# Kernel tuning notes

Hardware: AMD Instinct MI355X
Metric: run time of the kernel (lower is better)

The kernel has to match this reference:

```python
import jax, jax.numpy as jnp
import numpy as np

N_NODES = 100000
N_EDGES = 1600000
N_GRAPHS = 64
BN_EPS = 1e-5


def setup_inputs() -> dict:
    key = jax.random.key(0)
    ks = jax.random.split(key, 16)
    inp = {
        'x': jax.random.normal(ks[0], (N_NODES, 768), dtype=jnp.float32),
        'edge_index': jax.random.randint(ks[1], (2, N_EDGES), 0, N_NODES, dtype=jnp.int32),
        'batch': jnp.sort(jax.random.randint(ks[2], (N_NODES,), 0, N_GRAPHS, dtype=jnp.int32)),
        'W_in': jax.random.normal(ks[3], (768, 256), dtype=jnp.float32) * 0.02,
        'b_in': jax.random.normal(ks[4], (256,), dtype=jnp.float32) * 0.02,
        'W_g': jax.random.normal(ks[5], (3, 256, 256), dtype=jnp.float32) * 0.05,
        'b_g': jax.random.normal(ks[6], (3, 256), dtype=jnp.float32) * 0.02,
        'bn_gamma': jax.random.uniform(ks[7], (3, 256), dtype=jnp.float32) + 0.5,
        'bn_beta': jax.random.normal(ks[8], (3, 256), dtype=jnp.float32) * 0.02,
        'bn_mean': jax.random.normal(ks[9], (3, 256), dtype=jnp.float32) * 0.02,
        'bn_var': jax.random.uniform(ks[10], (3, 256), dtype=jnp.float32) + 0.5,
        'W1': jax.random.normal(ks[11], (256, 128), dtype=jnp.float32) * 0.06,
        'b1': jax.random.normal(ks[12], (128,), dtype=jnp.float32) * 0.02,
        'W2': jax.random.normal(ks[13], (128, 128), dtype=jnp.float32) * 0.08,
        'b2': jax.random.normal(ks[14], (128,), dtype=jnp.float32) * 0.02,
    }
    return inp


def reference(x, edge_index, batch, W_in, b_in, W_g, b_g, bn_gamma, bn_beta,
              bn_mean, bn_var, W1, b1, W2, b2):
    N = x.shape[0]
    # Add self loops (PyG GCNConv default)
    loop = jnp.arange(N, dtype=edge_index.dtype)
    src = jnp.concatenate([edge_index[0], loop])  # [E+N]
    dst = jnp.concatenate([edge_index[1], loop])
    # Symmetric GCN normalization: deg over dst after self loops
    deg = jax.ops.segment_sum(jnp.ones_like(src, dtype=x.dtype), dst, num_segments=N)
    dinv = jnp.where(deg > 0, jax.lax.rsqrt(deg), 0.0)
    norm = (dinv[src] * dinv[dst])[:, None]  # [E+N, 1]

    # input projection + relu
    h = jax.nn.relu(x @ W_in + b_in)  # [N, 256]

    for i in range(W_g.shape[0]):
        m = h @ W_g[i]                                   # [N, 256]
        agg = jax.ops.segment_sum(m[src] * norm, dst, num_segments=N) + b_g[i]
        # BatchNorm (eval mode, running stats)
        agg = (agg - bn_mean[i]) * (bn_gamma[i] * jax.lax.rsqrt(bn_var[i] + BN_EPS)) + bn_beta[i]
        h = jax.nn.relu(agg)  # dropout is identity in eval

    # global mean pool per graph
    sums = jax.ops.segment_sum(h, batch, num_segments=N_GRAPHS)       # [G, 256]
    cnts = jax.ops.segment_sum(jnp.ones((N,), x.dtype), batch, num_segments=N_GRAPHS)
    g = sums / jnp.maximum(cnts, 1.0)[:, None]

    # output MLP
    out = jax.nn.relu(g @ W1 + b1) @ W2 + b2  # [G, 128]
    return out
```

## Files before the change

kernel.cpp:

```cpp
#include <hip/hip_runtime.h>
#include <hip/hip_fp16.h>

#define HIDDEN 256

using hfrag = __attribute__((ext_vector_type(8))) _Float16;
using facc16 = __attribute__((ext_vector_type(16))) float;

#define BARRIER_LGKM()                                   \
  do {                                                   \
    asm volatile("s_waitcnt lgkmcnt(0)" ::: "memory");   \
    __builtin_amdgcn_s_barrier();                        \
  } while (0)

__device__ inline float h2f(unsigned short h) {
  return __half2float(__builtin_bit_cast(__half, h));
}
__device__ inline unsigned short f2h_bits(float v) {
  return __builtin_bit_cast(unsigned short, __float2half(v));
}
__device__ inline hfrag f2h8(const float4& a, const float4& b) {
  hfrag h;
  h[0] = (_Float16)a.x; h[1] = (_Float16)a.y;
  h[2] = (_Float16)a.z; h[3] = (_Float16)a.w;
  h[4] = (_Float16)b.x; h[5] = (_Float16)b.y;
  h[6] = (_Float16)b.z; h[7] = (_Float16)b.w;
  return h;
}

__global__ __launch_bounds__(256) void k_scan_a(const int* __restrict__ deg,
                                                int* __restrict__ bsum, int N) {
  const int t = threadIdx.x, lane = t & 63, w = t >> 6;
  const int idx = blockIdx.x * 256 + t;
  int x = (idx < N) ? deg[idx] : 0;
#pragma unroll
  for (int off = 32; off >= 1; off >>= 1) x += __shfl_xor(x, off);
  __shared__ int ws[4];
  if (lane == 0) ws[w] = x;
  __syncthreads();
  if (t == 0) bsum[blockIdx.x] = ws[0] + ws[1] + ws[2] + ws[3];
}

__global__ __launch_bounds__(512) void k_scan_b(const int* __restrict__ bsum,
                                                int* __restrict__ boff, int nb) {
  const int t = threadIdx.x, lane = t & 63, w = t >> 6;
  int orig = (t < nb) ? bsum[t] : 0;
  int x = orig;
#pragma unroll
  for (int off = 1; off < 64; off <<= 1) {
    int y = __shfl_up(x, off);
    if (lane >= off) x += y;
  }
  __shared__ int wsum[8];
  if (lane == 63) wsum[w] = x;
  __syncthreads();
  if (w == 0 && lane < 8) {
    int s = wsum[lane];
#pragma unroll
    for (int off = 1; off < 8; off <<= 1) {
      int y = __shfl_up(s, off);
      if (lane >= off) s += y;
    }
    wsum[lane] = s;
  }
  __syncthreads();
  int inc = x + (w > 0 ? wsum[w - 1] : 0);
  if (t < nb) boff[t] = inc - orig;
}

__global__ __launch_bounds__(256) void k_scan_c(const int* __restrict__ deg,
                                                const int* __restrict__ boff,
                                                int* __restrict__ row_ptr,
                                                float* __restrict__ dinv, int N) {
  const int t = threadIdx.x, lane = t & 63, w = t >> 6;
  const int idx = blockIdx.x * 256 + t;
  int d = (idx < N) ? deg[idx] : 0;
  int x = d;
#pragma unroll
  for (int off = 1; off < 64; off <<= 1) {
    int y = __shfl_up(x, off);
    if (lane >= off) x += y;
  }
  __shared__ int ws[4];
  if (lane == 63) ws[w] = x;
  __syncthreads();
  int add = boff[blockIdx.x];
#pragma unroll
  for (int j = 0; j < 4; ++j)
    if (j < w) add += ws[j];
  if (idx < N) {
    row_ptr[idx + 1] = x + add;
    dinv[idx] = 1.0f / sqrtf((float)d + 1.0f);
  }
  if (idx == 0) row_ptr[0] = 0;
}

__global__ __launch_bounds__(256) void k_prep_w(const float* __restrict__ W_in,
                                                const float* __restrict__ W_g,
                                                short* __restrict__ Wt) {
  const int e = blockIdx.x * blockDim.x + threadIdx.x;
  if (e >= 196608 + 3 * 65536) return;
  float v;
  int k, n;
  size_t base;
  if (e < 196608) {
    k = e >> 8;
    n = e & 255;
    v = W_in[e];
    base = 0;
  } else {
    int r = e - 196608;
    int lyr = r >> 16;
    k = (r >> 8) & 255;
    n = r & 255;
    v = W_g[r];
    base = 393216 + (size_t)lyr * 131072;
  }
  size_t pos = base + (size_t)(k >> 5) * 16384 + (size_t)n * 32 + (k & 31);
  __half hh = __float2half(v);
  float r2 = v - __half2float(hh);
  Wt[pos] = (short)__builtin_bit_cast(unsigned short, hh);
  Wt[pos + 8192] = (short)__builtin_bit_cast(unsigned short, __float2half(r2));
}

__device__ __forceinline__ void proj_body(int bx, const float* __restrict__ A,
                                          const short* __restrict__ Wt,
                                          const float* __restrict__ bias,
                                          unsigned short* __restrict__ Ch,
                                          int M, int K) {
  __shared__ short As[2][64][34];
  const int t = threadIdx.x;
  const int w = t >> 6, l = t & 63;
  const int g2 = l >> 5, l31 = l & 31;
  const int row0 = bx * 64;
  const int colbase = w * 64;
  const int arow = t >> 2, ak = (t & 3) << 3;

  facc16 acc[2][2];
#pragma unroll
  for (int i = 0; i < 2; ++i)
#pragma unroll
    for (int j = 0; j < 2; ++j) acc[i][j] = (facc16)(0.0f);

  const int nsteps = K >> 5;
  const int ga = row0 + arow;
  const bool aval = ga < M;
  const float* aptr = A + (size_t)ga * K + ak;

  float4 f0 = make_float4(0.f, 0.f, 0.f, 0.f), f1 = f0;
  if (aval) {
    f0 = *(const float4*)aptr;
    f1 = *(const float4*)(aptr + 4);
  }
  *(hfrag*)&As[0][arow][ak] = f2h8(f0, f1);
  if (nsteps > 1 && aval) {
    f0 = *(const float4*)(aptr + 32);
    f1 = *(const float4*)(aptr + 36);
  }

  int cur = 0;
  for (int s = 0; s < nsteps; ++s) {
    BARRIER_LGKM();
    hfrag bh[2][2], bl[2][2];
#pragma unroll
    for (int nt = 0; nt < 2; ++nt)
#pragma unroll
      for (int kh = 0; kh < 2; ++kh) {
        const short* wbp = Wt + ((size_t)s << 14) +
                           (size_t)(colbase + nt * 32 + l31) * 32 + kh * 16 + g2 * 8;
        bh[nt][kh] = *(const hfrag*)wbp;
        bl[nt][kh] = *(const hfrag*)(wbp + 8192);
      }
#pragma unroll
    for (int kh = 0; kh < 2; ++kh) {
      hfrag ah[2];
#pragma unroll
      for (int mt = 0; mt < 2; ++mt)
        ah[mt] = *(const hfrag*)&As[cur][mt * 32 + l31][kh * 16 + g2 * 8];
#pragma unroll
      for (int mt = 0; mt < 2; ++mt)
#pragma unroll
        for (int nt = 0; nt < 2; ++nt)
          acc[mt][nt] = __builtin_amdgcn_mfma_f32_32x32x16_f16(
              ah[mt], bh[nt][kh], acc[mt][nt], 0, 0, 0);
#pragma unroll
      for (int mt = 0; mt < 2; ++mt)
#pragma unroll
        for (int nt = 0; nt < 2; ++nt)
          acc[mt][nt] = __builtin_amdgcn_mfma_f32_32x32x16_f16(
              ah[mt], bl[nt][kh], acc[mt][nt], 0, 0, 0);
    }
    if (s + 1 < nsteps) {
      *(hfrag*)&As[cur ^ 1][arow][ak] = f2h8(f0, f1);
      if (s + 2 < nsteps && aval) {
        const float* ap = aptr + (size_t)(s + 2) * 32;
        f0 = *(const float4*)(ap + 0);
        f1 = *(const float4*)(ap + 4);
      }
    }
    cur ^= 1;
  }
#pragma unroll
  for (int nt = 0; nt < 2; ++nt) {
    const int col = colbase + nt * 32 + l31;
    const float b = bias[col];
#pragma unroll
    for (int mt = 0; mt < 2; ++mt)
#pragma unroll
      for (int r = 0; r < 16; ++r) {
        int row = row0 + mt * 32 + (r & 3) + 8 * (r >> 2) + 4 * g2;
        if (row < M)
          Ch[(size_t)row * HIDDEN + col] = f2h_bits(fmaxf(acc[mt][nt][r] + b, 0.f));
      }
  }
}

#define LG_LOAD(S, AA, BH, BL)                                          \
  {                                                                     \
    AA[0][0] = *(const hfrag*)(ap0 + (S) * 32);                         \
    AA[0][1] = *(const hfrag*)(ap0 + (S) * 32 + 16);                    \
    AA[1][0] = *(const hfrag*)(ap1 + (S) * 32);                         \
    AA[1][1] = *(const hfrag*)(ap1 + (S) * 32 + 16);                    \
    const short* wp = wb + ((size_t)(S) << 14);                         \
    BH[0][0] = *(const hfrag*)(wp);                                     \
    BH[0][1] = *(const hfrag*)(wp + 16);                                \
    BH[1][0] = *(const hfrag*)(wp + 1024);                              \
    BH[1][1] = *(const hfrag*)(wp + 1024 + 16);                         \
    BL[0][0] = *(const hfrag*)(wp + 8192);                              \
    BL[0][1] = *(const hfrag*)(wp + 8192 + 16);                         \
    BL[1][0] = *(const hfrag*)(wp + 8192 + 1024);                       \
    BL[1][1] = *(const hfrag*)(wp + 8192 + 1024 + 16);                  \
  }

#define LG_COMPUTE(AA, BH, BL)                                          \
  _Pragma("unroll") for (int kh = 0; kh < 2; ++kh) {                    \
    _Pragma("unroll") for (int mt = 0; mt < 2; ++mt)                    \
        _Pragma("unroll") for (int nt = 0; nt < 2; ++nt) acc[mt][nt] =  \
        __builtin_amdgcn_mfma_f32_32x32x16_f16(AA[mt][kh], BH[nt][kh],  \
                                               acc[mt][nt], 0, 0, 0);   \
    _Pragma("unroll") for (int mt = 0; mt < 2; ++mt)                    \
        _Pragma("unroll") for (int nt = 0; nt < 2; ++nt) acc[mt][nt] =  \
        __builtin_amdgcn_mfma_f32_32x32x16_f16(AA[mt][kh], BL[nt][kh],  \
                                               acc[mt][nt], 0, 0, 0);   \
  }

__device__ __forceinline__ void layer_gemm_body(
    int bx, const unsigned short* __restrict__ A, const short* __restrict__ Wt,
    const float* __restrict__ dinv, unsigned short* __restrict__ Cm, int M) {
  const int t = threadIdx.x;
  const int w = t >> 6, l = t & 63;
  const int g2 = l >> 5, l31 = l & 31;
  const int row0 = bx * 64;
  const int colbase = w * 64;

  facc16 acc[2][2];
#pragma unroll
  for (int i = 0; i < 2; ++i)
#pragma unroll
    for (int j = 0; j < 2; ++j) acc[i][j] = (facc16)(0.0f);

  int r0 = row0 + l31, r1 = row0 + 32 + l31;
  if (r0 >= M) r0 = M - 1;
  if (r1 >= M) r1 = M - 1;
  const unsigned short* ap0 = A + (size_t)r0 * HIDDEN + g2 * 8;
  const unsigned short* ap1 = A + (size_t)r1 * HIDDEN + g2 * 8;
  const short* wb = Wt + (size_t)(colbase + l31) * 32 + g2 * 8;

  hfrag aA[2][2], bhA[2][2], blA[2][2];
  hfrag aB[2][2], bhB[2][2], blB[2][2];

  LG_LOAD(0, aA, bhA, blA);
#pragma unroll
  for (int s = 0; s < 8; s += 2) {
    if (s + 1 < 8) LG_LOAD(s + 1, aB, bhB, blB);
    LG_COMPUTE(aA, bhA, blA);
    if (s + 2 < 8) LG_LOAD(s + 2, aA, bhA, blA);
    LG_COMPUTE(aB, bhB, blB);
  }
#pragma unroll
  for (int mt = 0; mt < 2; ++mt)
#pragma unroll
    for (int r = 0; r < 16; ++r) {
      int row = row0 + mt * 32 + (r & 3) + 8 * (r >> 2) + 4 * g2;
      if (row >= M) continue;
      const float sc = dinv[row];
#pragma unroll
      for (int nt = 0; nt < 2; ++nt)
        Cm[(size_t)row * HIDDEN + colbase + nt * 32 + l31] =
            f2h_bits(acc[mt][nt][r] * sc);
    }
}

__global__ __launch_bounds__(256, 3) void k_mega1(
    const float* __restrict__ x, const short* __restrict__ Wt,
    const float* __restrict__ b_in, unsigned short* __restrict__ h0, int M,
    int K, const int* __restrict__ dst, int* __restrict__ deg, int E,
    int ngemm, int nhist) {
  if ((int)blockIdx.x < ngemm) {
    proj_body(blockIdx.x, x, Wt, b_in, h0, M, K);
  } else {
    const int b = blockIdx.x - ngemm;
    for (int e = b * 256 + threadIdx.x; e < E; e += nhist * 256)
      atomicAdd(&deg[dst[e]], 1);
  }
}

__global__ __launch_bounds__(256, 2) void k_mega2(
    const unsigned short* __restrict__ h0, const short* __restrict__ WtL,
    const float* __restrict__ dinv, unsigned short* __restrict__ h1, int M,
    const int* __restrict__ src, const int* __restrict__ dst,
    const int* __restrict__ row_ptr, int* __restrict__ fill,
    int* __restrict__ csr, int E, int ngemm, int nfill) {
  if ((int)blockIdx.x < ngemm) {
    layer_gemm_body(blockIdx.x, h0, WtL, dinv, h1, M);
  } else {
    const int b = blockIdx.x - ngemm;
    for (int e = b * 256 + threadIdx.x; e < E; e += nfill * 256) {
      int d = dst[e];
      int pos = atomicAdd(&fill[d], 1);
      csr[row_ptr[d] + pos] = src[e];
    }
  }
}

__global__ __launch_bounds__(256, 2) void k_gemm_layer(
    const unsigned short* __restrict__ h, const short* __restrict__ WtL,
    const float* __restrict__ dinv, unsigned short* __restrict__ m, int M) {
  layer_gemm_body(blockIdx.x, h, WtL, dinv, m, M);
}

__global__ __launch_bounds__(256) void k_aggregate(
    const unsigned short* __restrict__ mp, const int* __restrict__ row_ptr,
    const int* __restrict__ csr, const float* __restrict__ dinv,
    const float* __restrict__ bg, const float* __restrict__ gamma,
    const float* __restrict__ beta, const float* __restrict__ mean,
    const float* __restrict__ var, unsigned short* __restrict__ hout, int N) {
  const int wave = threadIdx.x >> 6, l = threadIdx.x & 63;
  const int v = blockIdx.x * 4 + wave;
  if (v >= N) return;
  const int co = l << 2;
  ushort4 rs = *(const ushort4*)(mp + (size_t)v * HIDDEN + co);
  float4 acc;
  acc.x = h2f(rs.x); acc.y = h2f(rs.y); acc.z = h2f(rs.z); acc.w = h2f(rs.w);
  const int s = row_ptr[v], e = row_ptr[v + 1];
  int i = s;
  for (; i + 8 <= e; i += 8) {
    ushort4 r0 = *(const ushort4*)(mp + (size_t)csr[i + 0] * HIDDEN + co);
    ushort4 r1 = *(const ushort4*)(mp + (size_t)csr[i + 1] * HIDDEN + co);
    ushort4 r2 = *(const ushort4*)(mp + (size_t)csr[i + 2] * HIDDEN + co);
    ushort4 r3 = *(const ushort4*)(mp + (size_t)csr[i + 3] * HIDDEN + co);
    ushort4 r4 = *(const ushort4*)(mp + (size_t)csr[i + 4] * HIDDEN + co);
    ushort4 r5 = *(const ushort4*)(mp + (size_t)csr[i + 5] * HIDDEN + co);
    ushort4 r6 = *(const ushort4*)(mp + (size_t)csr[i + 6] * HIDDEN + co);
    ushort4 r7 = *(const ushort4*)(mp + (size_t)csr[i + 7] * HIDDEN + co);
    acc.x += h2f(r0.x) + h2f(r1.x) + h2f(r2.x) + h2f(r3.x) +
             h2f(r4.x) + h2f(r5.x) + h2f(r6.x) + h2f(r7.x);
    acc.y += h2f(r0.y) + h2f(r1.y) + h2f(r2.y) + h2f(r3.y) +
             h2f(r4.y) + h2f(r5.y) + h2f(r6.y) + h2f(r7.y);
    acc.z += h2f(r0.z) + h2f(r1.z) + h2f(r2.z) + h2f(r3.z) +
             h2f(r4.z) + h2f(r5.z) + h2f(r6.z) + h2f(r7.z);
    acc.w += h2f(r0.w) + h2f(r1.w) + h2f(r2.w) + h2f(r3.w) +
             h2f(r4.w) + h2f(r5.w) + h2f(r6.w) + h2f(r7.w);
  }
  for (; i < e; ++i) {
    ushort4 r0 = *(const ushort4*)(mp + (size_t)csr[i] * HIDDEN + co);
    acc.x += h2f(r0.x);
    acc.y += h2f(r0.y);
    acc.z += h2f(r0.z);
    acc.w += h2f(r0.w);
  }
  const float dv = dinv[v];
  float4 bg4 = *(const float4*)&bg[co];
  float4 g4 = *(const float4*)&gamma[co];
  float4 be4 = *(const float4*)&beta[co];
  float4 mn4 = *(const float4*)&mean[co];
  float4 vr4 = *(const float4*)&var[co];
  ushort4 o;
  o.x = f2h_bits(fmaxf((acc.x * dv + bg4.x - mn4.x) * (g4.x / sqrtf(vr4.x + 1e-5f)) + be4.x, 0.f));
  o.y = f2h_bits(fmaxf((acc.y * dv + bg4.y - mn4.y) * (g4.y / sqrtf(vr4.y + 1e-5f)) + be4.y, 0.f));
  o.z = f2h_bits(fmaxf((acc.z * dv + bg4.z - mn4.z) * (g4.z / sqrtf(vr4.z + 1e-5f)) + be4.z, 0.f));
  o.w = f2h_bits(fmaxf((acc.w * dv + bg4.w - mn4.w) * (g4.w / sqrtf(vr4.w + 1e-5f)) + be4.w, 0.f));
  *(ushort4*)&hout[(size_t)v * HIDDEN + co] = o;
}

__global__ __launch_bounds__(64) void k_count(const int* __restrict__ batch,
                                              float* __restrict__ cnt, int N,
                                              int G) {
  const int g = threadIdx.x;
  if (g >= G) return;
  int lo = 0, hi = N;
  while (lo < hi) {
    int mid = (lo + hi) >> 1;
    if (batch[mid] < g) lo = mid + 1; else hi = mid;
  }
  int lo2 = lo, hi2 = N;
  while (lo2 < hi2) {
    int mid = (lo2 + hi2) >> 1;
    if (batch[mid] < g + 1) lo2 = mid + 1; else hi2 = mid;
  }
  cnt[g] = (float)(lo2 - lo);
}

__global__ __launch_bounds__(256) void k_pool(const unsigned short* __restrict__ h,
                                              const int* __restrict__ batch,
                                              float* __restrict__ sums, int N) {
  const int t = threadIdx.x;
  const int start = blockIdx.x * 256;
  if (start >= N) return;
  const int end = min(start + 256, N);
  float acc = 0.f;
  int cur = batch[start];
  for (int n = start; n < end; ++n) {
    int g = batch[n];
    if (g != cur) {
      atomicAdd(&sums[cur * HIDDEN + t], acc);
      acc = 0.f;
      cur = g;
    }
    acc += h2f(h[(size_t)n * HIDDEN + t]);
  }
  atomicAdd(&sums[cur * HIDDEN + t], acc);
}

__global__ __launch_bounds__(128) void k_head(const float* __restrict__ sums,
                                              const float* __restrict__ cnt,
                                              const float* __restrict__ W1,
                                              const float* __restrict__ b1,
                                              const float* __restrict__ W2,
                                              const float* __restrict__ b2,
                                              float* __restrict__ out) {
  __shared__ float gr[256];
  __shared__ float t1[128];
  const int b = blockIdx.x, t = threadIdx.x;
  const float inv = 1.0f / fmaxf(cnt[b], 1.0f);
  gr[t] = sums[b * HIDDEN + t] * inv;
  gr[t + 128] = sums[b * HIDDEN + t + 128] * inv;
  __syncthreads();
  float a = b1[t];
  for (int k = 0; k < 256; ++k) a += gr[k] * W1[k * 128 + t];
  t1[t] = fmaxf(a, 0.f);
  __syncthreads();
  float o = b2[t];
  for (int k = 0; k < 128; ++k) o += t1[k] * W2[k * 128 + t];
  out[b * 128 + t] = o;
}

extern "C" void kernel_launch(void* const* d_in, const int* in_sizes, int n_in,
                              void* d_out, int out_size, void* d_ws,
                              size_t ws_size, hipStream_t stream) {
  (void)n_in;
  (void)ws_size;
  const float* x = (const float*)d_in[0];
  const int* ei = (const int*)d_in[1];
  const int* batch = (const int*)d_in[2];
  const float* W_in = (const float*)d_in[3];
  const float* b_in = (const float*)d_in[4];
  const float* W_g = (const float*)d_in[5];
  const float* b_g = (const float*)d_in[6];
  const float* bn_gamma = (const float*)d_in[7];
  const float* bn_beta = (const float*)d_in[8];
  const float* bn_mean = (const float*)d_in[9];
  const float* bn_var = (const float*)d_in[10];
  const float* W1 = (const float*)d_in[11];
  const float* b1 = (const float*)d_in[12];
  const float* W2 = (const float*)d_in[13];
  const float* b2 = (const float*)d_in[14];

  const int KIN = 768;
  const int N = in_sizes[0] / KIN;
  const int E = in_sizes[1] / 2;
  const int G = out_size / 128;

  const int* src = ei;
  const int* dst = ei + E;

  char* ws = (char*)d_ws;
  size_t off = 0;
  auto take = [&](size_t bytes) -> void* {
    void* p = ws + off;
    off += (bytes + 255) & ~(size_t)255;
    return p;
  };
  unsigned short* h0 = (unsigned short*)take((size_t)N * HIDDEN * 2);
  unsigned short* h1 = (unsigned short*)take((size_t)N * HIDDEN * 2);
  float* dinv = (float*)take((size_t)N * 4);
  int* deg = (int*)take((size_t)N * 4);
  int* fill = (int*)take((size_t)N * 4);
  int* row_ptr = (int*)take((size_t)(N + 1) * 4);
  int* csr = (int*)take((size_t)E * 4);
  float* sums = (float*)take((size_t)G * HIDDEN * 4);
  float* cnt = (float*)take((size_t)G * 4);
  short* Wt = (short*)take((size_t)(393216 + 3 * 131072) * 2);
  const int nb = (N + 255) / 256;
  int* bsum = (int*)take((size_t)nb * 4);
  int* boff = (int*)take((size_t)nb * 4);

  hipMemsetAsync(deg, 0, (size_t)N * 4, stream);
  hipMemsetAsync(fill, 0, (size_t)N * 4, stream);
  hipMemsetAsync(sums, 0, (size_t)G * HIDDEN * 4, stream);

  const int gx = (N + 63) / 64;
  const int NH = 256;
  const int NF = 256;

  k_prep_w<<<(196608 + 3 * 65536 + 255) / 256, 256, 0, stream>>>(W_in, W_g, Wt);
  k_mega1<<<gx + NH, 256, 0, stream>>>(x, Wt, b_in, h0, N, KIN, dst, deg, E,
                                       gx, NH);
  k_scan_a<<<nb, 256, 0, stream>>>(deg, bsum, N);
  k_scan_b<<<1, 512, 0, stream>>>(bsum, boff, nb);
  k_scan_c<<<nb, 256, 0, stream>>>(deg, boff, row_ptr, dinv, N);
  k_mega2<<<gx + NF, 256, 0, stream>>>(h0, Wt + 393216, dinv, h1, N, src, dst,
                                       row_ptr, fill, csr, E, gx, NF);
  k_aggregate<<<(N + 3) / 4, 256, 0, stream>>>(
      h1, row_ptr, csr, dinv, b_g, bn_gamma, bn_beta, bn_mean, bn_var, h0, N);
  for (int i = 1; i < 3; ++i) {
    k_gemm_layer<<<gx, 256, 0, stream>>>(h0, Wt + 393216 + (size_t)i * 131072,
                                         dinv, h1, N);
    k_aggregate<<<(N + 3) / 4, 256, 0, stream>>>(
        h1, row_ptr, csr, dinv, b_g + i * HIDDEN, bn_gamma + i * HIDDEN,
        bn_beta + i * HIDDEN, bn_mean + i * HIDDEN, bn_var + i * HIDDEN, h0, N);
  }
  k_count<<<1, 64, 0, stream>>>(batch, cnt, N, G);
  k_pool<<<(N + 255) / 256, 256, 0, stream>>>(h0, batch, sums, N);
  k_head<<<G, 128, 0, stream>>>(sums, cnt, W1, b1, W2, b2, (float*)d_out);
}
```

Before: 974.9 us.

## Drop LDS staging in input projection; load x straight into MFMA fragments

The input projection GEMM no longer stages x through shared memory with a barrier every K-step. Each lane now loads its fp32 rows of x straight from global memory into registers, converts them to fp16 fragments, and double-buffers both A and B across a fully unrolled 24-step K loop. This removes the LDS round trip and the per-step barriers. In exchange it uses many more registers (raw float4 buffers for two stages), so launch bounds drop from 3 to 2 blocks per CU, which lowers occupancy. Each wave also loads x rows redundantly, since every one of the four waves reads the same A rows.

```diff
diff --git a/kernel.cpp b/kernel.cpp
--- a/kernel.cpp
+++ b/kernel.cpp
@@ -5,12 +5,6 @@
 
 using hfrag = __attribute__((ext_vector_type(8))) _Float16;
 using facc16 = __attribute__((ext_vector_type(16))) float;
-
-#define BARRIER_LGKM()                                   \
-  do {                                                   \
-    asm volatile("s_waitcnt lgkmcnt(0)" ::: "memory");   \
-    __builtin_amdgcn_s_barrier();                        \
-  } while (0)
 
 __device__ inline float h2f(unsigned short h) {
   return __half2float(__builtin_bit_cast(__half, h));
@@ -122,104 +116,8 @@
   Wt[pos + 8192] = (short)__builtin_bit_cast(unsigned short, __float2half(r2));
 }
 
-__device__ __forceinline__ void proj_body(int bx, const float* __restrict__ A,
-                                          const short* __restrict__ Wt,
-                                          const float* __restrict__ bias,
-                                          unsigned short* __restrict__ Ch,
-                                          int M, int K) {
-  __shared__ short As[2][64][34];
-  const int t = threadIdx.x;
-  const int w = t >> 6, l = t & 63;
-  const int g2 = l >> 5, l31 = l & 31;
-  const int row0 = bx * 64;
-  const int colbase = w * 64;
-  const int arow = t >> 2, ak = (t & 3) << 3;
-
-  facc16 acc[2][2];
-#pragma unroll
-  for (int i = 0; i < 2; ++i)
-#pragma unroll
-    for (int j = 0; j < 2; ++j) acc[i][j] = (facc16)(0.0f);
-
-  const int nsteps = K >> 5;
-  const int ga = row0 + arow;
-  const bool aval = ga < M;
-  const float* aptr = A + (size_t)ga * K + ak;
-
-  float4 f0 = make_float4(0.f, 0.f, 0.f, 0.f), f1 = f0;
-  if (aval) {
-    f0 = *(const float4*)aptr;
-    f1 = *(const float4*)(aptr + 4);
-  }
-  *(hfrag*)&As[0][arow][ak] = f2h8(f0, f1);
-  if (nsteps > 1 && aval) {
-    f0 = *(const float4*)(aptr + 32);
-    f1 = *(const float4*)(aptr + 36);
-  }
-
-  int cur = 0;
-  for (int s = 0; s < nsteps; ++s) {
-    BARRIER_LGKM();
-    hfrag bh[2][2], bl[2][2];
-#pragma unroll
-    for (int nt = 0; nt < 2; ++nt)
-#pragma unroll
-      for (int kh = 0; kh < 2; ++kh) {
-        const short* wbp = Wt + ((size_t)s << 14) +
-                           (size_t)(colbase + nt * 32 + l31) * 32 + kh * 16 + g2 * 8;
-        bh[nt][kh] = *(const hfrag*)wbp;
-        bl[nt][kh] = *(const hfrag*)(wbp + 8192);
-      }
-#pragma unroll
-    for (int kh = 0; kh < 2; ++kh) {
-      hfrag ah[2];
-#pragma unroll
-      for (int mt = 0; mt < 2; ++mt)
-        ah[mt] = *(const hfrag*)&As[cur][mt * 32 + l31][kh * 16 + g2 * 8];
-#pragma unroll
-      for (int mt = 0; mt < 2; ++mt)
-#pragma unroll
-        for (int nt = 0; nt < 2; ++nt)
-          acc[mt][nt] = __builtin_amdgcn_mfma_f32_32x32x16_f16(
-              ah[mt], bh[nt][kh], acc[mt][nt], 0, 0, 0);
-#pragma unroll
-      for (int mt = 0; mt < 2; ++mt)
-#pragma unroll
-        for (int nt = 0; nt < 2; ++nt)
-          acc[mt][nt] = __builtin_amdgcn_mfma_f32_32x32x16_f16(
-              ah[mt], bl[nt][kh], acc[mt][nt], 0, 0, 0);
-    }
-    if (s + 1 < nsteps) {
-      *(hfrag*)&As[cur ^ 1][arow][ak] = f2h8(f0, f1);
-      if (s + 2 < nsteps && aval) {
-        const float* ap = aptr + (size_t)(s + 2) * 32;
-        f0 = *(const float4*)(ap + 0);
-        f1 = *(const float4*)(ap + 4);
-      }
-    }
-    cur ^= 1;
-  }
-#pragma unroll
-  for (int nt = 0; nt < 2; ++nt) {
-    const int col = colbase + nt * 32 + l31;
-    const float b = bias[col];
-#pragma unroll
-    for (int mt = 0; mt < 2; ++mt)
-#pragma unroll
-      for (int r = 0; r < 16; ++r) {
-        int row = row0 + mt * 32 + (r & 3) + 8 * (r >> 2) + 4 * g2;
-        if (row < M)
-          Ch[(size_t)row * HIDDEN + col] = f2h_bits(fmaxf(acc[mt][nt][r] + b, 0.f));
-      }
-  }
-}
-
-#define LG_LOAD(S, AA, BH, BL)                                          \
+#define B_LOAD(S, BH, BL)                                               \
   {                                                                     \
-    AA[0][0] = *(const hfrag*)(ap0 + (S) * 32);                         \
-    AA[0][1] = *(const hfrag*)(ap0 + (S) * 32 + 16);                    \
-    AA[1][0] = *(const hfrag*)(ap1 + (S) * 32);                         \
-    AA[1][1] = *(const hfrag*)(ap1 + (S) * 32 + 16);                    \
     const short* wp = wb + ((size_t)(S) << 14);                         \
     BH[0][0] = *(const hfrag*)(wp);                                     \
     BH[0][1] = *(const hfrag*)(wp + 16);                                \
@@ -231,7 +129,7 @@
     BL[1][1] = *(const hfrag*)(wp + 8192 + 1024 + 16);                  \
   }
 
-#define LG_COMPUTE(AA, BH, BL)                                          \
+#define TILE_COMPUTE(AA, BH, BL)                                        \
   _Pragma("unroll") for (int kh = 0; kh < 2; ++kh) {                    \
     _Pragma("unroll") for (int mt = 0; mt < 2; ++mt)                    \
         _Pragma("unroll") for (int nt = 0; nt < 2; ++nt) acc[mt][nt] =  \
@@ -243,6 +141,101 @@
                                                acc[mt][nt], 0, 0, 0);   \
   }
 
+#define PR_LOADA(S, RAW)                                  \
+  {                                                       \
+    RAW[0] = *(const float4*)(xp0 + (S) * 32);            \
+    RAW[1] = *(const float4*)(xp0 + (S) * 32 + 4);        \
+    RAW[2] = *(const float4*)(xp0 + (S) * 32 + 16);       \
+    RAW[3] = *(const float4*)(xp0 + (S) * 32 + 20);       \
+    RAW[4] = *(const float4*)(xp1 + (S) * 32);            \
+    RAW[5] = *(const float4*)(xp1 + (S) * 32 + 4);        \
+    RAW[6] = *(const float4*)(xp1 + (S) * 32 + 16);       \
+    RAW[7] = *(const float4*)(xp1 + (S) * 32 + 20);       \
+  }
+
+#define PR_CVT(RAW, HF)                 \
+  {                                     \
+    HF[0][0] = f2h8(RAW[0], RAW[1]);    \
+    HF[0][1] = f2h8(RAW[2], RAW[3]);    \
+    HF[1][0] = f2h8(RAW[4], RAW[5]);    \
+    HF[1][1] = f2h8(RAW[6], RAW[7]);    \
+  }
+
+__device__ __forceinline__ void proj_body(int bx, const float* __restrict__ A,
+                                          const short* __restrict__ Wt,
+                                          const float* __restrict__ bias,
+                                          unsigned short* __restrict__ Ch,
+                                          int M, int K) {
+  const int t = threadIdx.x;
+  const int w = t >> 6, l = t & 63;
+  const int g2 = l >> 5, l31 = l & 31;
+  const int row0 = bx * 64;
+  const int colbase = w * 64;
+
+  facc16 acc[2][2];
+#pragma unroll
+  for (int i = 0; i < 2; ++i)
+#pragma unroll
+    for (int j = 0; j < 2; ++j) acc[i][j] = (facc16)(0.0f);
+
+  int r0 = row0 + l31, r1 = row0 + 32 + l31;
+  if (r0 >= M) r0 = M - 1;
+  if (r1 >= M) r1 = M - 1;
+  const float* xp0 = A + (size_t)r0 * K + g2 * 8;
+  const float* xp1 = A + (size_t)r1 * K + g2 * 8;
+  const short* wb = Wt + (size_t)(colbase + l31) * 32 + g2 * 8;
+
+  float4 rawA[8], rawB[8];
+  hfrag hfA[2][2], hfB[2][2];
+  hfrag bhA[2][2], blA[2][2], bhB[2][2], blB[2][2];
+
+  PR_LOADA(0, rawA);
+  B_LOAD(0, bhA, blA);
+  PR_CVT(rawA, hfA);
+  PR_LOADA(1, rawB);
+  B_LOAD(1, bhB, blB);
+
+#pragma unroll
+  for (int s = 0; s < 24; s += 2) {
+    TILE_COMPUTE(hfA, bhA, blA);
+    PR_CVT(rawB, hfB);
+    if (s + 2 < 24) {
+      PR_LOADA(s + 2, rawA);
+      B_LOAD(s + 2, bhA, blA);
+    }
+    TILE_COMPUTE(hfB, bhB, blB);
+    if (s + 2 < 24) {
+      PR_CVT(rawA, hfA);
+      if (s + 3 < 24) {
+        PR_LOADA(s + 3, rawB);
+        B_LOAD(s + 3, bhB, blB);
+      }
+    }
+  }
+#pragma unroll
+  for (int nt = 0; nt < 2; ++nt) {
+    const int col = colbase + nt * 32 + l31;
+    const float b = bias[col];
+#pragma unroll
+    for (int mt = 0; mt < 2; ++mt)
+#pragma unroll
+      for (int r = 0; r < 16; ++r) {
+        int row = row0 + mt * 32 + (r & 3) + 8 * (r >> 2) + 4 * g2;
+        if (row < M)
+          Ch[(size_t)row * HIDDEN + col] = f2h_bits(fmaxf(acc[mt][nt][r] + b, 0.f));
+      }
+  }
+}
+
+#define LG_LOAD(S, AA, BH, BL)                                          \
+  {                                                                     \
+    AA[0][0] = *(const hfrag*)(ap0 + (S) * 32);                         \
+    AA[0][1] = *(const hfrag*)(ap0 + (S) * 32 + 16);                    \
+    AA[1][0] = *(const hfrag*)(ap1 + (S) * 32);                         \
+    AA[1][1] = *(const hfrag*)(ap1 + (S) * 32 + 16);                    \
+    B_LOAD(S, BH, BL);                                                  \
+  }
+
 __device__ __forceinline__ void layer_gemm_body(
     int bx, const unsigned short* __restrict__ A, const short* __restrict__ Wt,
     const float* __restrict__ dinv, unsigned short* __restrict__ Cm, int M) {
@@ -272,9 +265,9 @@
 #pragma unroll
   for (int s = 0; s < 8; s += 2) {
     if (s + 1 < 8) LG_LOAD(s + 1, aB, bhB, blB);
-    LG_COMPUTE(aA, bhA, blA);
+    TILE_COMPUTE(aA, bhA, blA);
     if (s + 2 < 8) LG_LOAD(s + 2, aA, bhA, blA);
-    LG_COMPUTE(aB, bhB, blB);
+    TILE_COMPUTE(aB, bhB, blB);
   }
 #pragma unroll
   for (int mt = 0; mt < 2; ++mt)
@@ -290,7 +283,7 @@
     }
 }
 
-__global__ __launch_bounds__(256, 3) void k_mega1(
+__global__ __launch_bounds__(256, 2) void k_mega1(
     const float* __restrict__ x, const short* __restrict__ Wt,
     const float* __restrict__ b_in, unsigned short* __restrict__ h0, int M,
     int K, const int* __restrict__ dst, int* __restrict__ deg, int E,
```

Result: slower. 1.078 ms (+10.5%).
